# Kernel tuning notes

Hardware: AMD Instinct MI355X
Metric: run time of the kernel (lower is better)

## Reference

```python
import jax, jax.numpy as jnp
import numpy as np

DIM = 128
WINDOW_TOKENS = 64  # window_size**2 = 8*8


def _conv3x3(x, w):
    # x: [B,C,H,W], w: [O,I,3,3], padding=1 (SAME)
    return jax.lax.conv_general_dilated(
        x, w, window_strides=(1, 1), padding='SAME',
        dimension_numbers=('NCHW', 'OIHW', 'NCHW'))


def _pixel_shuffle2(x):
    # torch.nn.PixelShuffle(2): [B, C*4, H, W] -> [B, C, 2H, 2W]
    B, C4, H, W = x.shape
    C = C4 // 4
    x = x.reshape(B, C, 2, 2, H, W)
    x = x.transpose(0, 1, 4, 2, 5, 3)  # [B, C, H, 2, W, 2]
    return x.reshape(B, C, H * 2, W * 2)


def setup_inputs() -> dict:
    key = jax.random.key(0)
    ks = jax.random.split(key, 12)
    B, C = 4, DIM
    f0 = jax.random.normal(ks[0], (B, C, 64, 64), jnp.float32)
    f1 = jax.random.normal(ks[1], (B, C, 128, 128), jnp.float32)
    f2 = jax.random.normal(ks[2], (B, C, 256, 256), jnp.float32)
    s = 0.02
    # Linear weights stored as [in, out] so forward is x @ W
    Wq = jax.random.normal(ks[3], (C, C), jnp.float32) * s
    Wk = jax.random.normal(ks[4], (C, C), jnp.float32) * s
    Wv = jax.random.normal(ks[5], (C, C), jnp.float32) * s
    Wql = jax.random.normal(ks[6], (C, C), jnp.float32) * s
    Wkl = jax.random.normal(ks[7], (C, C), jnp.float32) * s
    Wvl = jax.random.normal(ks[8], (C, C), jnp.float32) * s
    gate_w = jax.random.normal(ks[9], (2 * C, C), jnp.float32) * s
    conv0 = jax.random.normal(ks[10], (4 * C, C, 3, 3), jnp.float32) * s
    conv1 = jax.random.normal(ks[11], (4 * C, C, 3, 3), jnp.float32) * s
    return dict(f0=f0, f1=f1, f2=f2, Wq=Wq, Wk=Wk, Wv=Wv,
                Wql=Wql, Wkl=Wkl, Wvl=Wvl, gate_w=gate_w,
                conv0=conv0, conv1=conv1)


def reference(f0, f1, f2, Wq, Wk, Wv, Wql, Wkl, Wvl, gate_w, conv0, conv1):
    feats = (f0, f1, f2)
    B, C = f0.shape[0], f0.shape[1]
    scale = C ** (-0.5)
    # flatten+concat: [B, N, C]
    toks = [f.reshape(B, C, -1).transpose(0, 2, 1) for f in feats]
    x = jnp.concatenate(toks, axis=1)
    N = x.shape[1]
    wt = WINDOW_TOKENS
    nw = N // wt  # N is divisible by wt for these shapes (no padding)
    windows = x.reshape(B, nw, wt, C)

    # ---- global path (mode='center'): attention over window means ----
    centers = windows.mean(axis=2)  # [B, nw, C]
    Q = centers @ Wq
    K = centers @ Wk
    V = centers @ Wv
    attn = jax.nn.softmax(jnp.einsum('bnc,bmc->bnm', Q, K) * scale, axis=-1)
    y_centers = jnp.einsum('bnm,bmc->bnc', attn, V) * centers
    y_global = jnp.broadcast_to(y_centers[:, :, None, :], (B, nw, wt, C)).reshape(B, N, C)

    # ---- local path: attention within each window (batched over windows) ----
    Ql = windows @ Wql
    Kl = windows @ Wkl
    Vl = windows @ Wvl
    attn_l = jax.nn.softmax(jnp.einsum('bwqc,bwkc->bwqk', Ql, Kl) * scale, axis=-1)
    y_local = (jnp.einsum('bwqk,bwkc->bwqc', attn_l, Vl) * windows).reshape(B, N, C)

    # ---- gated fusion ----
    alpha = jax.nn.sigmoid(jnp.concatenate([y_global, y_local], axis=-1) @ gate_w)
    y = alpha * y_global + (1.0 - alpha) * y_local

    # ---- reshape back to feature maps ----
    maps = []
    start = 0
    for f in feats:
        H, W = f.shape[2], f.shape[3]
        cnt = H * W
        maps.append(y[:, start:start + cnt, :].transpose(0, 2, 1).reshape(B, C, H, W))
        start += cnt
    # ---- inverse wavelet reconstruction (conv3x3 -> pixel shuffle -> add) ----
    outputs = [maps[0]]
    z = maps[0]
    z = _pixel_shuffle2(_conv3x3(z, conv0)) + maps[1]
    outputs.append(z)
    z = _pixel_shuffle2(_conv3x3(z, conv1)) + maps[2]
    outputs.append(z)
    return tuple(outputs)
```

## Files before the change

kernel.cpp:

```cpp
#include <hip/hip_runtime.h>
#include <math.h>

#define WT 64
#define NWIN 1344
#define NP 1408
#define SROW_STRIDE 1352
constexpr float SCALE = 0.088388347648318447f;

#define OUT0 0
#define OUT1 2097152
#define OUT2 10485760

typedef __attribute__((ext_vector_type(8))) short bfrag;
typedef __attribute__((ext_vector_type(8))) _Float16 hfrag;
typedef __attribute__((ext_vector_type(4))) float f32x4;

#define MFMA16 __builtin_amdgcn_mfma_f32_16x16x32_bf16
#define MFMA16H __builtin_amdgcn_mfma_f32_16x16x32_f16

__device__ __forceinline__ unsigned short f2b(float f) {
    union { float f; unsigned u; } v; v.f = f;
    unsigned r = v.u + 0x7fffu + ((v.u >> 16) & 1u);
    return (unsigned short)(r >> 16);
}
__device__ __forceinline__ float b2f(unsigned short u) {
    union { unsigned u; float f; } v; v.u = ((unsigned)u) << 16; return v.f;
}
__device__ __forceinline__ int pack2(float a, float b) {
    return (int)f2b(a) | ((int)f2b(b) << 16);
}

__device__ __forceinline__ bfrag ld256(const char* region, int row, int k) {
    int off = (2 * k) ^ ((row & 7) << 4);
    return *(const bfrag*)(region + row * 256 + off);
}
__device__ __forceinline__ bfrag ld128(const char* region, int row, int k) {
    int off = (2 * k) ^ ((row & 7) << 4);
    return *(const bfrag*)(region + row * 128 + off);
}

__global__ void k_prep(const float* __restrict__ Wql, const float* __restrict__ Wkl,
                       const float* __restrict__ Wvl, const float* __restrict__ gw,
                       const float* __restrict__ Wq, const float* __restrict__ Wk,
                       const float* __restrict__ Wv,
                       unsigned short* __restrict__ MtB,
                       unsigned short* __restrict__ WvltB,
                       unsigned short* __restrict__ G1tB,
                       unsigned short* __restrict__ G0tB,
                       unsigned short* __restrict__ MgtB,
                       unsigned short* __restrict__ WvtB) {
    int n = blockIdx.x, k = threadIdx.x;
    if (blockIdx.y == 0) {
        float a = 0.f;
        for (int c = 0; c < 128; ++c) a += Wkl[n * 128 + c] * Wql[k * 128 + c];
        MtB[n * 128 + k] = f2b(a);
    } else if (blockIdx.y == 1) {
        WvltB[n * 128 + k] = f2b(Wvl[k * 128 + n]);
    } else if (blockIdx.y == 2) {
        G1tB[n * 128 + k] = f2b(gw[(128 + k) * 128 + n]);
    } else if (blockIdx.y == 3) {
        G0tB[n * 128 + k] = f2b(gw[k * 128 + n]);
    } else if (blockIdx.y == 4) {
        float a = 0.f;
        for (int c = 0; c < 128; ++c) a += Wk[n * 128 + c] * Wq[k * 128 + c];
        MgtB[n * 128 + k] = f2b(a);
    } else {
        WvtB[n * 128 + k] = f2b(Wv[k * 128 + n]);
    }
}

__global__ __launch_bounds__(256) void k_prep_conv(
    const float* __restrict__ w0, const float* __restrict__ w1,
    _Float16* __restrict__ W0, _Float16* __restrict__ W1) {
    int idx = blockIdx.x * 256 + threadIdx.x;
    const float* w = blockIdx.y ? w1 : w0;
    _Float16* o = blockIdx.y ? W1 : W0;
    int slice = idx >> 14, rem = idx & 16383;
    int oc = rem >> 5, k = rem & 31;
    int ics = slice / 9, tap = slice - ics * 9;
    o[idx] = (_Float16)w[((size_t)oc * 128 + ics * 32 + k) * 9 + tap];
}

__device__ __forceinline__ void window_src(int n0, const float* f0, const float* f1,
                                           const float* f2, const float*& f, int& p0,
                                           int& HW, int& obase) {
    if (n0 < 4096)        { f = f0; p0 = n0;          HW = 4096;  obase = OUT0; }
    else if (n0 < 20480)  { f = f1; p0 = n0 - 4096;   HW = 16384; obase = OUT1; }
    else                  { f = f2; p0 = n0 - 20480;  HW = 65536; obase = OUT2; }
}

__global__ __launch_bounds__(256) void k_centers(
    const float* __restrict__ f0, const float* __restrict__ f1,
    const float* __restrict__ f2, float* __restrict__ ctr,
    unsigned short* __restrict__ ctrb) {
    int w = blockIdx.x, b = blockIdx.y;
    const float* f; int p0, HW, ob;
    window_src(w * WT, f0, f1, f2, f, p0, HW, ob);
    int lane = threadIdx.x & 63, cg = threadIdx.x >> 6;
    for (int c = cg; c < 128; c += 4) {
        float v = f[(b * 128 + c) * HW + p0 + lane];
        #pragma unroll
        for (int off = 32; off; off >>= 1) v += __shfl_xor(v, off);
        if (lane == 0) {
            float mv = v * (1.0f / 64.0f);
            ctr[(b * NWIN + w) * 128 + c] = mv;
            ctrb[(b * NWIN + w) * 128 + c] = f2b(mv);
        }
    }
}

__global__ __launch_bounds__(256) void k_vg(
    const unsigned short* __restrict__ ctrb, const unsigned short* __restrict__ WvtB,
    unsigned short* __restrict__ Vgt) {
    int blk = blockIdx.x, b = blockIdx.y;
    int mb = blk * 32;
    int tid = threadIdx.x, wid = tid >> 6, lane = tid & 63;
    int lr = lane & 15, lg = lane >> 4;
    int nb = wid * 32;
    f32x4 vg[2][2] = {};
    const unsigned short* Cb = ctrb + ((size_t)b * NWIN + mb) * 128;
    #pragma unroll
    for (int ks = 0; ks < 4; ++ks) {
        int k = ks * 32 + lg * 8;
        bfrag b0 = *(const bfrag*)(Cb + lr * 128 + k);
        bfrag b1 = *(const bfrag*)(Cb + (16 + lr) * 128 + k);
        bfrag v0 = *(const bfrag*)(WvtB + (nb + lr) * 128 + k);
        bfrag v1 = *(const bfrag*)(WvtB + (nb + 16 + lr) * 128 + k);
        vg[0][0] = MFMA16(v0, b0, vg[0][0], 0, 0, 0);
        vg[0][1] = MFMA16(v0, b1, vg[0][1], 0, 0, 0);
        vg[1][0] = MFMA16(v1, b0, vg[1][0], 0, 0, 0);
        vg[1][1] = MFMA16(v1, b1, vg[1][1], 0, 0, 0);
    }
    #pragma unroll
    for (int ni = 0; ni < 2; ++ni)
        #pragma unroll
        for (int mj = 0; mj < 2; ++mj) {
            int n0 = nb + ni * 16 + 4 * lg;
            int m = mb + mj * 16 + lr;
            #pragma unroll
            for (int r = 0; r < 4; ++r)
                Vgt[((size_t)b * 128 + n0 + r) * NP + m] = f2b(vg[ni][mj][r]);
        }
}

#define QKPV_LDS (32 * SROW_STRIDE * 2 + 8192)

__global__ __launch_bounds__(256, 1) void k_qkpv(
    const unsigned short* __restrict__ ctrb, const unsigned short* __restrict__ MgtB,
    const unsigned short* __restrict__ Vgt, const unsigned short* __restrict__ G0tB,
    const float* __restrict__ ctr, float* __restrict__ ycen,
    float* __restrict__ g0g) {
    extern __shared__ char smem2[];
    unsigned short* Srow = (unsigned short*)smem2;
    char* Ys = smem2 + 32 * SROW_STRIDE * 2;
    __shared__ float mxs[32], invs[32];
    int blk = blockIdx.x, b = blockIdx.y;
    int mb = blk * 32;
    int tid = threadIdx.x, wid = tid >> 6, lane = tid & 63;
    int lr = lane & 15, lg = lane >> 4;

    {
        int nb = wid * 32;
        f32x4 tg[2][2] = {};
        const unsigned short* Cb = ctrb + ((size_t)b * NWIN + mb) * 128;
        #pragma unroll
        for (int ks = 0; ks < 4; ++ks) {
            int k = ks * 32 + lg * 8;
            bfrag b0 = *(const bfrag*)(Cb + lr * 128 + k);
            bfrag b1 = *(const bfrag*)(Cb + (16 + lr) * 128 + k);
            bfrag m0 = *(const bfrag*)(MgtB + (nb + lr) * 128 + k);
            bfrag m1 = *(const bfrag*)(MgtB + (nb + 16 + lr) * 128 + k);
            tg[0][0] = MFMA16(m0, b0, tg[0][0], 0, 0, 0);
            tg[0][1] = MFMA16(m0, b1, tg[0][1], 0, 0, 0);
            tg[1][0] = MFMA16(m1, b0, tg[1][0], 0, 0, 0);
            tg[1][1] = MFMA16(m1, b1, tg[1][1], 0, 0, 0);
        }
        #pragma unroll
        for (int ni = 0; ni < 2; ++ni)
            #pragma unroll
            for (int mj = 0; mj < 2; ++mj) {
                int n0 = nb + ni * 16 + 4 * lg;
                int m = mj * 16 + lr;
                int2 v; v.x = pack2(tg[ni][mj][0], tg[ni][mj][1]);
                v.y = pack2(tg[ni][mj][2], tg[ni][mj][3]);
                *(int2*)(Ys + m * 256 + ((2 * n0) ^ ((m & 7) << 4))) = v;
            }
    }
    __syncthreads();

    {
        int wm = (wid & 1) * 16, wn = (wid >> 1) * 32;
        for (int tile = 0; tile < 21; ++tile) {
            int nb = tile * 64 + wn;
            f32x4 acc[2] = {};
            #pragma unroll
            for (int ks = 0; ks < 4; ++ks) {
                int k = ks * 32 + lg * 8;
                bfrag a = ld256(Ys, wm + lr, k);
                #pragma unroll
                for (int nt = 0; nt < 2; ++nt) {
                    bfrag bb = *(const bfrag*)(ctrb + ((size_t)b * NWIN + nb + nt * 16 + lr) * 128 + k);
                    acc[nt] = MFMA16(a, bb, acc[nt], 0, 0, 0);
                }
            }
            #pragma unroll
            for (int nt = 0; nt < 2; ++nt) {
                int col = nb + nt * 16 + lr;
                #pragma unroll
                for (int r = 0; r < 4; ++r)
                    Srow[(wm + 4 * lg + r) * SROW_STRIDE + col] = f2b(acc[nt][r]);
            }
        }
    }
    __syncthreads();

    {
        int row = tid >> 3, sub = tid & 7;
        const unsigned short* sr = Srow + row * SROW_STRIDE;
        float mx = -1e30f;
        for (int c = sub; c < 1344; c += 8) mx = fmaxf(mx, b2f(sr[c]));
        mx = fmaxf(mx, __shfl_xor(mx, 1));
        mx = fmaxf(mx, __shfl_xor(mx, 2));
        mx = fmaxf(mx, __shfl_xor(mx, 4));
        float sum = 0.f;
        for (int c = sub; c < 1344; c += 8) sum += __expf((b2f(sr[c]) - mx) * SCALE);
        sum += __shfl_xor(sum, 1);
        sum += __shfl_xor(sum, 2);
        sum += __shfl_xor(sum, 4);
        if (sub == 0) { mxs[row] = mx; invs[row] = 1.0f / sum; }
    }
    __syncthreads();
    for (int idx = tid; idx < 32 * (SROW_STRIDE / 8); idx += 256) {
        int row = idx / (SROW_STRIDE / 8), c8 = idx % (SROW_STRIDE / 8);
        float mx = mxs[row], inv = invs[row];
        unsigned short* sp = Srow + row * SROW_STRIDE + c8 * 8;
        unsigned short o[8];
        #pragma unroll
        for (int e = 0; e < 8; ++e) {
            int c = c8 * 8 + e;
            float p = (c < 1344) ? __expf((b2f(sp[e]) - mx) * SCALE) * inv : 0.f;
            o[e] = f2b(p);
        }
        *(int4*)sp = *(int4*)o;
    }
    __syncthreads();

    {
        int cb = wid * 32;
        f32x4 acc[2][2] = {};
        const unsigned short* Vb = Vgt + (size_t)b * 128 * NP;
        for (int it = 0; it < 42; ++it) {
            int k = it * 32 + lg * 8;
            bfrag a0 = *(const bfrag*)(Vb + (size_t)(cb + lr) * NP + k);
            bfrag a1 = *(const bfrag*)(Vb + (size_t)(cb + 16 + lr) * NP + k);
            bfrag b0 = *(const bfrag*)(Srow + lr * SROW_STRIDE + k);
            bfrag b1 = *(const bfrag*)(Srow + (16 + lr) * SROW_STRIDE + k);
            acc[0][0] = MFMA16(a0, b0, acc[0][0], 0, 0, 0);
            acc[0][1] = MFMA16(a0, b1, acc[0][1], 0, 0, 0);
            acc[1][0] = MFMA16(a1, b0, acc[1][0], 0, 0, 0);
            acc[1][1] = MFMA16(a1, b1, acc[1][1], 0, 0, 0);
        }
        #pragma unroll
        for (int ci = 0; ci < 2; ++ci)
            #pragma unroll
            for (int mj = 0; mj < 2; ++mj) {
                int c0 = cb + ci * 16 + 4 * lg;
                int mr = mj * 16 + lr;
                int m = mb + mr;
                size_t base = ((size_t)b * NWIN + m) * 128 + c0;
                float4 cv = *(const float4*)(ctr + base);
                float4 y;
                y.x = acc[ci][mj][0] * cv.x;
                y.y = acc[ci][mj][1] * cv.y;
                y.z = acc[ci][mj][2] * cv.z;
                y.w = acc[ci][mj][3] * cv.w;
                *(float4*)(ycen + base) = y;
                int2 pv; pv.x = pack2(y.x, y.y); pv.y = pack2(y.z, y.w);
                *(int2*)(Ys + mr * 256 + ((2 * c0) ^ ((mr & 7) << 4))) = pv;
            }
    }
    __syncthreads();

    {
        int nb = wid * 32;
        f32x4 g[2][2] = {};
        #pragma unroll
        for (int ks = 0; ks < 4; ++ks) {
            int k = ks * 32 + lg * 8;
            bfrag a0 = *(const bfrag*)(G0tB + (nb + lr) * 128 + k);
            bfrag a1 = *(const bfrag*)(G0tB + (nb + 16 + lr) * 128 + k);
            bfrag b0 = ld256(Ys, lr, k);
            bfrag b1 = ld256(Ys, 16 + lr, k);
            g[0][0] = MFMA16(a0, b0, g[0][0], 0, 0, 0);
            g[0][1] = MFMA16(a0, b1, g[0][1], 0, 0, 0);
            g[1][0] = MFMA16(a1, b0, g[1][0], 0, 0, 0);
            g[1][1] = MFMA16(a1, b1, g[1][1], 0, 0, 0);
        }
        #pragma unroll
        for (int ni = 0; ni < 2; ++ni)
            #pragma unroll
            for (int mj = 0; mj < 2; ++mj) {
                int m = mb + mj * 16 + lr;
                int n0 = nb + ni * 16 + 4 * lg;
                #pragma unroll
                for (int r = 0; r < 4; ++r)
                    g0g[((size_t)b * NWIN + m) * 128 + n0 + r] = g[ni][mj][r];
            }
    }
}

#define XB_OFF 0
#define WT_OFF 16384
#define XM_OFF 49152
#define VT_OFF 65536
#define SMEM_SZ 81920

__global__ __launch_bounds__(256, 2) void k_local_mfma(
    const float* __restrict__ f0, const float* __restrict__ f1,
    const float* __restrict__ f2,
    const unsigned short* __restrict__ MtB,
    const unsigned short* __restrict__ WvltB,
    const unsigned short* __restrict__ G1tB,
    const float* __restrict__ g0g, const float* __restrict__ ycen,
    float* __restrict__ out) {
    extern __shared__ char smem[];
    char* Xb = smem + XB_OFF;
    char* Wt = smem + WT_OFF;
    char* XMb = smem + XM_OFF;
    char* Vt = smem + VT_OFF;

    int w = blockIdx.x, b = blockIdx.y;
    const float* f; int p0, HW, obase;
    window_src(w * WT, f0, f1, f2, f, p0, HW, obase);

    int tid = threadIdx.x;
    int wid = tid >> 6, lane = tid & 63;
    int lr = lane & 15, lg = lane >> 4;

    {
        int t0 = tid & 63, cq = tid >> 6;
        const float* src = f + (size_t)(b * 128 + cq * 32) * HW + p0 + t0;
        float xv[32];
        #pragma unroll
        for (int i = 0; i < 32; ++i) xv[i] = src[(size_t)i * HW];
        int4 wreg[8];
        const int4* wsrc = (const int4*)MtB;
        #pragma unroll
        for (int j = 0; j < 8; ++j) wreg[j] = wsrc[j * 256 + tid];
        #pragma unroll
        for (int j = 0; j < 4; ++j) {
            int c0 = cq * 32 + j * 8;
            int4 v;
            v.x = pack2(xv[j * 8 + 0], xv[j * 8 + 1]);
            v.y = pack2(xv[j * 8 + 2], xv[j * 8 + 3]);
            v.z = pack2(xv[j * 8 + 4], xv[j * 8 + 5]);
            v.w = pack2(xv[j * 8 + 6], xv[j * 8 + 7]);
            *(int4*)(Xb + t0 * 256 + ((2 * c0) ^ ((t0 & 7) << 4))) = v;
        }
        #pragma unroll
        for (int j = 0; j < 8; ++j) {
            int ci = j * 256 + tid, n = ci >> 4, pos = ci & 15;
            *(int4*)(Wt + n * 256 + ((pos * 16) ^ ((n & 7) << 4))) = wreg[j];
        }
    }
    __syncthreads();

    int t = 16 * wid + lr;

    {
        f32x4 acc[8] = {};
        #pragma unroll
        for (int ks = 0; ks < 4; ++ks) {
            int k = ks * 32 + lg * 8;
            bfrag xb = ld256(Xb, t, k);
            #pragma unroll
            for (int ct = 0; ct < 8; ++ct) {
                bfrag am = ld256(Wt, 16 * ct + lr, k);
                acc[ct] = MFMA16(am, xb, acc[ct], 0, 0, 0);
            }
        }
        #pragma unroll
        for (int ct = 0; ct < 8; ++ct) {
            int c0 = 16 * ct + 4 * lg;
            int2 v; v.x = pack2(acc[ct][0], acc[ct][1]); v.y = pack2(acc[ct][2], acc[ct][3]);
            *(int2*)(XMb + t * 256 + ((2 * c0) ^ ((t & 7) << 4))) = v;
        }
    }
    __syncthreads();

    {
        int4 wreg[8];
        const int4* wsrc = (const int4*)WvltB;
        #pragma unroll
        for (int j = 0; j < 8; ++j) wreg[j] = wsrc[j * 256 + tid];

        f32x4 s[4] = {};
        #pragma unroll
        for (int ks = 0; ks < 4; ++ks) {
            int k = ks * 32 + lg * 8;
            bfrag bxm = ld256(XMb, t, k);
            #pragma unroll
            for (int ut = 0; ut < 4; ++ut) {
                bfrag ax = ld256(Xb, 16 * ut + lr, k);
                s[ut] = MFMA16(ax, bxm, s[ut], 0, 0, 0);
            }
        }
        float m = -1e30f;
        #pragma unroll
        for (int ut = 0; ut < 4; ++ut)
            #pragma unroll
            for (int r = 0; r < 4; ++r) m = fmaxf(m, s[ut][r]);
        m = fmaxf(m, __shfl_xor(m, 16));
        m = fmaxf(m, __shfl_xor(m, 32));
        float sum = 0.f;
        float e[4][4];
        #pragma unroll
        for (int ut = 0; ut < 4; ++ut)
            #pragma unroll
            for (int r = 0; r < 4; ++r) {
                e[ut][r] = __expf((s[ut][r] - m) * SCALE);
                sum += e[ut][r];
            }
        sum += __shfl_xor(sum, 16);
        sum += __shfl_xor(sum, 32);
        float pinv = 1.0f / sum;
        #pragma unroll
        for (int ut = 0; ut < 4; ++ut) {
            int u0 = 16 * ut + 4 * lg;
            int2 v;
            v.x = pack2(e[ut][0] * pinv, e[ut][1] * pinv);
            v.y = pack2(e[ut][2] * pinv, e[ut][3] * pinv);
            *(int2*)(XMb + t * 256 + ((2 * u0) ^ ((t & 7) << 4))) = v;
        }
        #pragma unroll
        for (int j = 0; j < 8; ++j) {
            int ci = j * 256 + tid, n = ci >> 4, pos = ci & 15;
            *(int4*)(Wt + n * 256 + ((pos * 16) ^ ((n & 7) << 4))) = wreg[j];
        }
    }
    __syncthreads();

    int4 wregG[8];
    {
        const int4* wsrc = (const int4*)G1tB;
        #pragma unroll
        for (int j = 0; j < 8; ++j) wregG[j] = wsrc[j * 256 + tid];

        f32x4 vacc[8] = {};
        #pragma unroll
        for (int ks = 0; ks < 4; ++ks) {
            int k = ks * 32 + lg * 8;
            bfrag ax = ld256(Xb, t, k);
            #pragma unroll
            for (int ct = 0; ct < 8; ++ct) {
                bfrag bw = ld256(Wt, 16 * ct + lr, k);
                vacc[ct] = MFMA16(ax, bw, vacc[ct], 0, 0, 0);
            }
        }
        #pragma unroll
        for (int ct = 0; ct < 8; ++ct) {
            int c = 16 * ct + lr;
            int u0 = 16 * wid + 4 * lg;
            int2 v; v.x = pack2(vacc[ct][0], vacc[ct][1]); v.y = pack2(vacc[ct][2], vacc[ct][3]);
            *(int2*)(Vt + c * 128 + ((2 * u0) ^ ((c & 7) << 4))) = v;
        }
    }
    __syncthreads();

    float yl[8][4];
    float4 yg4[8], g04[8];
    {
        #pragma unroll
        for (int j = 0; j < 8; ++j) {
            int ci = j * 256 + tid, n = ci >> 4, pos = ci & 15;
            *(int4*)(Wt + n * 256 + ((pos * 16) ^ ((n & 7) << 4))) = wregG[j];
        }
        size_t rbase = ((size_t)b * NWIN + w) * 128 + 4 * lg;
        #pragma unroll
        for (int nt = 0; nt < 8; ++nt) {
            yg4[nt] = *(const float4*)(ycen + rbase + 16 * nt);
            g04[nt] = *(const float4*)(g0g + rbase + 16 * nt);
        }
        f32x4 y[8] = {};
        #pragma unroll
        for (int us = 0; us < 2; ++us) {
            int u = us * 32 + lg * 8;
            bfrag bp = ld256(XMb, t, u);
            #pragma unroll
            for (int ct = 0; ct < 8; ++ct) {
                bfrag av = ld128(Vt, 16 * ct + lr, u);
                y[ct] = MFMA16(av, bp, y[ct], 0, 0, 0);
            }
        }
        #pragma unroll
        for (int ct = 0; ct < 8; ++ct) {
            int c0 = 16 * ct + 4 * lg;
            int2 xw = *(const int2*)(Xb + t * 256 + ((2 * c0) ^ ((t & 7) << 4)));
            float x0 = b2f((unsigned short)(xw.x & 0xffff));
            float x1 = b2f((unsigned short)((unsigned)xw.x >> 16));
            float x2 = b2f((unsigned short)(xw.y & 0xffff));
            float x3 = b2f((unsigned short)((unsigned)xw.y >> 16));
            yl[ct][0] = y[ct][0] * x0;
            yl[ct][1] = y[ct][1] * x1;
            yl[ct][2] = y[ct][2] * x2;
            yl[ct][3] = y[ct][3] * x3;
            int2 v; v.x = pack2(yl[ct][0], yl[ct][1]); v.y = pack2(yl[ct][2], yl[ct][3]);
            *(int2*)(Xb + t * 256 + ((2 * c0) ^ ((t & 7) << 4))) = v;
        }
    }
    __syncthreads();

    {
        f32x4 g[8] = {};
        #pragma unroll
        for (int ks = 0; ks < 4; ++ks) {
            int k = ks * 32 + lg * 8;
            bfrag byl = ld256(Xb, t, k);
            #pragma unroll
            for (int nt = 0; nt < 8; ++nt) {
                bfrag ag = ld256(Wt, 16 * nt + lr, k);
                g[nt] = MFMA16(ag, byl, g[nt], 0, 0, 0);
            }
        }
        #pragma unroll
        for (int nt = 0; nt < 8; ++nt) {
            float gv[4] = {g04[nt].x, g04[nt].y, g04[nt].z, g04[nt].w};
            float yv4[4] = {yg4[nt].x, yg4[nt].y, yg4[nt].z, yg4[nt].w};
            #pragma unroll
            for (int r = 0; r < 4; ++r) {
                int c = 16 * nt + 4 * lg + r;
                float a = 1.0f / (1.0f + __expf(-(g[nt][r] + gv[r])));
                float yv = a * yv4[r] + (1.0f - a) * yl[nt][r];
                out[obase + (size_t)(b * 128 + c) * HW + p0 + t] = yv;
            }
        }
    }
}

template <int H, int W>
__global__ __launch_bounds__(256, 2) void k_conv_mfma(
    const float* __restrict__ in, const _Float16* __restrict__ Wcv,
    float* __restrict__ out) {
    constexpr int TXN = W / 32;
    int tile = blockIdx.x;
    int ty = tile / TXN, tx = tile % TXN;
    int y0 = ty * 4, x0 = tx * 32;
    int ob = blockIdx.y * 256;
    int b = blockIdx.z;

    __shared__ __align__(16) char sXs[16384];

    int tid = threadIdx.x;
    int wid = tid >> 6, lane = tid & 63;
    int lr = lane & 15, lg = lane >> 4;

    f32x4 acc[8][4] = {};

    int sy = tid / 34, sx = tid - sy * 34;
    int gy = y0 + sy - 1, gx = x0 + sx - 1;
    bool act = tid < 204;
    bool ok = act && gy >= 0 && gy < H && gx >= 0 && gx < W;
    const float* gp = in + (size_t)b * 128 * H * W + (size_t)gy * W + gx;
    int xswz = (tid >> 3) & 1;

    const _Float16* wbase = Wcv + (size_t)(ob + lr) * 32 + lg * 8;

    hfrag afC[4], afN[4];
    #pragma unroll
    for (int n = 0; n < 4; ++n)
        afC[n] = *(const hfrag*)(wbase + (size_t)(wid * 4 + n) * 512);

    if (act) {
        float xv[32];
        if (ok) {
            #pragma unroll
            for (int ic = 0; ic < 32; ++ic) xv[ic] = gp[(size_t)ic * H * W];
        } else {
            #pragma unroll
            for (int ic = 0; ic < 32; ++ic) xv[ic] = 0.f;
        }
        #pragma unroll
        for (int s = 0; s < 4; ++s) {
            _Float16 hh[8];
            #pragma unroll
            for (int e = 0; e < 8; ++e) hh[e] = (_Float16)xv[s * 8 + e];
            *(int4*)(sXs + tid * 80 + ((s ^ xswz) << 4)) = *(int4*)hh;
        }
    }
    __syncthreads();

    for (int ics = 0; ics < 4; ++ics) {
        if (ics) {
            __syncthreads();
            if (act) {
                float xv[32];
                if (ok) {
                    #pragma unroll
                    for (int ic = 0; ic < 32; ++ic)
                        xv[ic] = gp[(size_t)(ics * 32 + ic) * H * W];
                } else {
                    #pragma unroll
                    for (int ic = 0; ic < 32; ++ic) xv[ic] = 0.f;
                }
                #pragma unroll
                for (int s = 0; s < 4; ++s) {
                    _Float16 hh[8];
                    #pragma unroll
                    for (int e = 0; e < 8; ++e) hh[e] = (_Float16)xv[s * 8 + e];
                    *(int4*)(sXs + tid * 80 + ((s ^ xswz) << 4)) = *(int4*)hh;
                }
            }
            __syncthreads();
        }
        #pragma unroll
        for (int tap = 0; tap < 9; ++tap) {
            int kg = ics * 9 + tap;
            if (tap < 8 || ics < 3) {
                const _Float16* ws = wbase + (size_t)(kg + 1) * 16384;
                #pragma unroll
                for (int n = 0; n < 4; ++n)
                    afN[n] = *(const hfrag*)(ws + (size_t)(wid * 4 + n) * 512);
            }
            int dy = tap / 3, dx = tap - dy * 3;
            hfrag bf[8];
            #pragma unroll
            for (int m = 0; m < 8; ++m) {
                int row = ((m >> 1) + dy) * 34 + (m & 1) * 16 + lr + dx;
                bf[m] = *(const hfrag*)(sXs + row * 80 + ((lg ^ ((row >> 3) & 1)) << 4));
            }
            #pragma unroll
            for (int m = 0; m < 8; ++m)
                #pragma unroll
                for (int n = 0; n < 4; ++n)
                    acc[m][n] = MFMA16H(afC[n], bf[m], acc[m][n], 0, 0, 0);
            #pragma unroll
            for (int n = 0; n < 4; ++n) afC[n] = afN[n];
        }
    }

    float* outb = out + (size_t)b * 128 * 4 * H * W;
    #pragma unroll
    for (int n = 0; n < 4; ++n) {
        int oc0 = ob + (wid * 4 + n) * 16 + lg * 4;
        int c = oc0 >> 2;
        #pragma unroll
        for (int mr = 0; mr < 4; ++mr) {
            int py = y0 + mr;
            #pragma unroll
            for (int i2 = 0; i2 < 2; ++i2) {
                size_t rowb = ((size_t)c * (2 * H) + 2 * py + i2) * (2 * W);
                float2* p0 = (float2*)(outb + rowb + 2 * (x0 + lr));
                float2 v0 = *p0;
                v0.x += acc[2 * mr][n][i2 * 2 + 0];
                v0.y += acc[2 * mr][n][i2 * 2 + 1];
                *p0 = v0;
                float2* p1 = (float2*)(outb + rowb + 2 * (x0 + 16 + lr));
                float2 v1 = *p1;
                v1.x += acc[2 * mr + 1][n][i2 * 2 + 0];
                v1.y += acc[2 * mr + 1][n][i2 * 2 + 1];
                *p1 = v1;
            }
        }
    }
}

extern "C" void kernel_launch(void* const* d_in, const int* in_sizes, int n_in,
                              void* d_out, int out_size, void* d_ws, size_t ws_size,
                              hipStream_t stream) {
    const float* f0 = (const float*)d_in[0];
    const float* f1 = (const float*)d_in[1];
    const float* f2 = (const float*)d_in[2];
    const float* Wq = (const float*)d_in[3];
    const float* Wk = (const float*)d_in[4];
    const float* Wv = (const float*)d_in[5];
    const float* Wql = (const float*)d_in[6];
    const float* Wkl = (const float*)d_in[7];
    const float* Wvl = (const float*)d_in[8];
    const float* gate_w = (const float*)d_in[9];
    const float* conv0 = (const float*)d_in[10];
    const float* conv1 = (const float*)d_in[11];
    float* out = (float*)d_out;
    float* ws = (float*)d_ws;

    float* ctr = ws;
    float* ycen = ctr + 688128;
    float* g0g = ycen + 688128;
    unsigned short* MtB = (unsigned short*)(g0g + 688128);
    unsigned short* WvltB = MtB + 16384;
    unsigned short* G1tB = WvltB + 16384;
    unsigned short* G0tB = G1tB + 16384;
    unsigned short* MgtB = G0tB + 16384;
    unsigned short* WvtB = MgtB + 16384;
    _Float16* Wcv0 = (_Float16*)(WvtB + 16384);
    _Float16* Wcv1 = Wcv0 + 589824;
    unsigned short* ctrb = (unsigned short*)(Wcv1 + 589824);
    unsigned short* Vgt = ctrb + 688128;

    hipFuncSetAttribute((const void*)k_local_mfma,
                        hipFuncAttributeMaxDynamicSharedMemorySize, SMEM_SZ);
    hipFuncSetAttribute((const void*)k_qkpv,
                        hipFuncAttributeMaxDynamicSharedMemorySize, QKPV_LDS);

    k_prep<<<dim3(128, 6), 128, 0, stream>>>(Wql, Wkl, Wvl, gate_w, Wq, Wk, Wv,
                                             MtB, WvltB, G1tB, G0tB, MgtB, WvtB);
    k_prep_conv<<<dim3(2304, 2), 256, 0, stream>>>(conv0, conv1, Wcv0, Wcv1);
    k_centers<<<dim3(NWIN, 4), 256, 0, stream>>>(f0, f1, f2, ctr, ctrb);
    k_vg<<<dim3(NWIN / 32, 4), 256, 0, stream>>>(ctrb, WvtB, Vgt);
    k_qkpv<<<dim3(NWIN / 32, 4), 256, QKPV_LDS, stream>>>(
        ctrb, MgtB, Vgt, G0tB, ctr, ycen, g0g);
    k_local_mfma<<<dim3(NWIN, 4), 256, SMEM_SZ, stream>>>(
        f0, f1, f2, MtB, WvltB, G1tB, g0g, ycen, out);
    k_conv_mfma<64, 64><<<dim3(32, 2, 4), 256, 0, stream>>>(out + OUT0, Wcv0, out + OUT1);
    k_conv_mfma<128, 128><<<dim3(128, 2, 4), 256, 0, stream>>>(out + OUT1, Wcv1, out + OUT2);
}
```

Before: 549.4 us.

## Merge weight-prep kernels and split conv output channels across more blocks

Two prep kernels are merged into one launch, so the bf16 weight transforms ride in extra grid rows beside the fp16 conv weight repack, saving one launch. The conv kernel now computes 128 output channels per block instead of 256, which halves accumulator registers and doubles the grid along the channel dimension, and launch bounds are raised to 3 blocks per CU. More, smaller blocks should improve occupancy and fill more CUs on the smaller conv. The cost is that each input tile is loaded and converted to fp16 twice as often.

```diff
diff --git a/kernel.cpp b/kernel.cpp
--- a/kernel.cpp
+++ b/kernel.cpp
@@ -39,46 +39,46 @@
     return *(const bfrag*)(region + row * 128 + off);
 }
 
-__global__ void k_prep(const float* __restrict__ Wql, const float* __restrict__ Wkl,
-                       const float* __restrict__ Wvl, const float* __restrict__ gw,
-                       const float* __restrict__ Wq, const float* __restrict__ Wk,
-                       const float* __restrict__ Wv,
-                       unsigned short* __restrict__ MtB,
-                       unsigned short* __restrict__ WvltB,
-                       unsigned short* __restrict__ G1tB,
-                       unsigned short* __restrict__ G0tB,
-                       unsigned short* __restrict__ MgtB,
-                       unsigned short* __restrict__ WvtB) {
-    int n = blockIdx.x, k = threadIdx.x;
-    if (blockIdx.y == 0) {
+__global__ __launch_bounds__(256) void k_prep_all(
+    const float* __restrict__ w0, const float* __restrict__ w1,
+    _Float16* __restrict__ W0, _Float16* __restrict__ W1,
+    const float* __restrict__ Wql, const float* __restrict__ Wkl,
+    const float* __restrict__ Wvl, const float* __restrict__ gw,
+    const float* __restrict__ Wq, const float* __restrict__ Wk,
+    const float* __restrict__ Wv,
+    unsigned short* __restrict__ MtB, unsigned short* __restrict__ WvltB,
+    unsigned short* __restrict__ G1tB, unsigned short* __restrict__ G0tB,
+    unsigned short* __restrict__ MgtB, unsigned short* __restrict__ WvtB) {
+    if (blockIdx.y < 2) {
+        int idx = blockIdx.x * 256 + threadIdx.x;
+        const float* w = blockIdx.y ? w1 : w0;
+        _Float16* o = blockIdx.y ? W1 : W0;
+        int slice = idx >> 14, rem = idx & 16383;
+        int oc = rem >> 5, k = rem & 31;
+        int ics = slice / 9, tap = slice - ics * 9;
+        o[idx] = (_Float16)w[((size_t)oc * 128 + ics * 32 + k) * 9 + tap];
+        return;
+    }
+    if (blockIdx.x >= 384) return;
+    int idx = blockIdx.x * 256 + threadIdx.x;
+    int k = idx & 127, n = (idx >> 7) & 127, v = idx >> 14;
+    if (v == 0) {
         float a = 0.f;
         for (int c = 0; c < 128; ++c) a += Wkl[n * 128 + c] * Wql[k * 128 + c];
         MtB[n * 128 + k] = f2b(a);
-    } else if (blockIdx.y == 1) {
+    } else if (v == 1) {
         WvltB[n * 128 + k] = f2b(Wvl[k * 128 + n]);
-    } else if (blockIdx.y == 2) {
+    } else if (v == 2) {
         G1tB[n * 128 + k] = f2b(gw[(128 + k) * 128 + n]);
-    } else if (blockIdx.y == 3) {
+    } else if (v == 3) {
         G0tB[n * 128 + k] = f2b(gw[k * 128 + n]);
-    } else if (blockIdx.y == 4) {
+    } else if (v == 4) {
         float a = 0.f;
         for (int c = 0; c < 128; ++c) a += Wk[n * 128 + c] * Wq[k * 128 + c];
         MgtB[n * 128 + k] = f2b(a);
     } else {
         WvtB[n * 128 + k] = f2b(Wv[k * 128 + n]);
     }
-}
-
-__global__ __launch_bounds__(256) void k_prep_conv(
-    const float* __restrict__ w0, const float* __restrict__ w1,
-    _Float16* __restrict__ W0, _Float16* __restrict__ W1) {
-    int idx = blockIdx.x * 256 + threadIdx.x;
-    const float* w = blockIdx.y ? w1 : w0;
-    _Float16* o = blockIdx.y ? W1 : W0;
-    int slice = idx >> 14, rem = idx & 16383;
-    int oc = rem >> 5, k = rem & 31;
-    int ics = slice / 9, tap = slice - ics * 9;
-    o[idx] = (_Float16)w[((size_t)oc * 128 + ics * 32 + k) * 9 + tap];
 }
 
 __device__ __forceinline__ void window_src(int n0, const float* f0, const float* f1,
@@ -538,14 +538,14 @@
 }
 
 template <int H, int W>
-__global__ __launch_bounds__(256, 2) void k_conv_mfma(
+__global__ __launch_bounds__(256, 3) void k_conv_mfma(
     const float* __restrict__ in, const _Float16* __restrict__ Wcv,
     float* __restrict__ out) {
     constexpr int TXN = W / 32;
     int tile = blockIdx.x;
     int ty = tile / TXN, tx = tile % TXN;
     int y0 = ty * 4, x0 = tx * 32;
-    int ob = blockIdx.y * 256;
+    int ob = blockIdx.y * 128;
     int b = blockIdx.z;
 
     __shared__ __align__(16) char sXs[16384];
@@ -554,7 +554,7 @@
     int wid = tid >> 6, lane = tid & 63;
     int lr = lane & 15, lg = lane >> 4;
 
-    f32x4 acc[8][4] = {};
+    f32x4 acc[8][2] = {};
 
     int sy = tid / 34, sx = tid - sy * 34;
     int gy = y0 + sy - 1, gx = x0 + sx - 1;
@@ -565,10 +565,10 @@
 
     const _Float16* wbase = Wcv + (size_t)(ob + lr) * 32 + lg * 8;
 
-    hfrag afC[4], afN[4];
+    hfrag afC[2], afN[2];
     #pragma unroll
-    for (int n = 0; n < 4; ++n)
-        afC[n] = *(const hfrag*)(wbase + (size_t)(wid * 4 + n) * 512);
+    for (int n = 0; n < 2; ++n)
+        afC[n] = *(const hfrag*)(wbase + (size_t)(wid * 2 + n) * 512);
 
     if (act) {
         float xv[32];
@@ -618,8 +618,8 @@
             if (tap < 8 || ics < 3) {
                 const _Float16* ws = wbase + (size_t)(kg + 1) * 16384;
                 #pragma unroll
-                for (int n = 0; n < 4; ++n)
-                    afN[n] = *(const hfrag*)(ws + (size_t)(wid * 4 + n) * 512);
+                for (int n = 0; n < 2; ++n)
+                    afN[n] = *(const hfrag*)(ws + (size_t)(wid * 2 + n) * 512);
             }
             int dy = tap / 3, dx = tap - dy * 3;
             hfrag bf[8];
@@ -631,17 +631,17 @@
             #pragma unroll
             for (int m = 0; m < 8; ++m)
                 #pragma unroll
-                for (int n = 0; n < 4; ++n)
+                for (int n = 0; n < 2; ++n)
                     acc[m][n] = MFMA16H(afC[n], bf[m], acc[m][n], 0, 0, 0);
             #pragma unroll
-            for (int n = 0; n < 4; ++n) afC[n] = afN[n];
+            for (int n = 0; n < 2; ++n) afC[n] = afN[n];
         }
     }
 
     float* outb = out + (size_t)b * 128 * 4 * H * W;
     #pragma unroll
-    for (int n = 0; n < 4; ++n) {
-        int oc0 = ob + (wid * 4 + n) * 16 + lg * 4;
+    for (int n = 0; n < 2; ++n) {
+        int oc0 = ob + (wid * 2 + n) * 16 + lg * 4;
         int c = oc0 >> 2;
         #pragma unroll
         for (int mr = 0; mr < 4; ++mr) {
@@ -701,15 +701,15 @@
     hipFuncSetAttribute((const void*)k_qkpv,
                         hipFuncAttributeMaxDynamicSharedMemorySize, QKPV_LDS);
 
-    k_prep<<<dim3(128, 6), 128, 0, stream>>>(Wql, Wkl, Wvl, gate_w, Wq, Wk, Wv,
-                                             MtB, WvltB, G1tB, G0tB, MgtB, WvtB);
-    k_prep_conv<<<dim3(2304, 2), 256, 0, stream>>>(conv0, conv1, Wcv0, Wcv1);
+    k_prep_all<<<dim3(2304, 3), 256, 0, stream>>>(
+        conv0, conv1, Wcv0, Wcv1, Wql, Wkl, Wvl, gate_w, Wq, Wk, Wv,
+        MtB, WvltB, G1tB, G0tB, MgtB, WvtB);
     k_centers<<<dim3(NWIN, 4), 256, 0, stream>>>(f0, f1, f2, ctr, ctrb);
     k_vg<<<dim3(NWIN / 32, 4), 256, 0, stream>>>(ctrb, WvtB, Vgt);
     k_qkpv<<<dim3(NWIN / 32, 4), 256, QKPV_LDS, stream>>>(
         ctrb, MgtB, Vgt, G0tB, ctr, ycen, g0g);
     k_local_mfma<<<dim3(NWIN, 4), 256, SMEM_SZ, stream>>>(
         f0, f1, f2, MtB, WvltB, G1tB, g0g, ycen, out);
-    k_conv_mfma<64, 64><<<dim3(32, 2, 4), 256, 0, stream>>>(out + OUT0, Wcv0, out + OUT1);
-    k_conv_mfma<128, 128><<<dim3(128, 2, 4), 256, 0, stream>>>(out + OUT1, Wcv1, out + OUT2);
-}
+    k_conv_mfma<64, 64><<<dim3(32, 4, 4), 256, 0, stream>>>(out + OUT0, Wcv0, out + OUT1);
+    k_conv_mfma<128, 128><<<dim3(128, 4, 4), 256, 0, stream>>>(out + OUT1, Wcv1, out + OUT2);
+}
```

Result: faster. 529.6 us (-3.6%).
